# Kernel optimization log

Hardware: AMD Instinct MI355X
Metric: run time of the kernel (lower is better)

The kernel has to match this reference:

```python
import jax, jax.numpy as jnp
import numpy as np

# FlowNetC correlation hyperparameters (init_kwargs)
PAD = 4            # pad_size
KERNEL = 1         # kernel_size (1x1 patch)
MD = 4             # max_displacement
STRIDE1 = 1        # stride over output positions
STRIDE2 = 1        # stride over displacements


def setup_inputs() -> dict:
    key = jax.random.key(0)
    k1, k2 = jax.random.split(key)
    input1 = jax.random.normal(k1, (8, 256, 96, 128), dtype=jnp.float32)
    input2 = jax.random.normal(k2, (8, 256, 96, 128), dtype=jnp.float32)
    return {"input1": input1, "input2": input2}


def reference(input1, input2):
    # Cost volume: out[b, d, y, x] = (1/C) * sum_c input1[b,c,y,x] * input2[b,c,y+dy,x+dx]
    # for all displacements (dy, dx) in [-MD, MD] with step STRIDE2.
    # With pad_size == max_displacement, kernel_size == 1, stride1 == 1 the output
    # spatial grid equals the input grid (FlowNetC configuration). Normalization
    # matches correlation_cuda: sumelems = kernel_size^2 * C.
    B, C, H, W = input1.shape
    p2 = jnp.pad(input2, ((0, 0), (0, 0), (PAD, PAD), (PAD, PAD)))
    disp = range(-MD, MD + 1, STRIDE2)  # 9 offsets -> 81 displacement channels
    outs = []
    for dy in disp:
        for dx in disp:
            shifted = jax.lax.dynamic_slice(p2, (0, 0, PAD + dy, PAD + dx), (B, C, H, W))
            # mean over channels == sum / (KERNEL*KERNEL*C) since KERNEL == 1
            outs.append(jnp.mean(input1 * shifted, axis=1))
    return jnp.stack(outs, axis=1)  # [B, 81, H, W]
```

## Files before the change

kernel.cpp:

```cpp
#include <hip/hip_runtime.h>
#include <hip/hip_bf16.h>


#define B_ 8
#define C_ 256
#define H_ 96
#define W_ 128
#define HW_ 12288
#define CHW_ 3145728

#define IN1_OFF 0
#define IN2_OFF 16384
#define IN2_ROWB (48 * 64)

typedef __attribute__((ext_vector_type(8))) short short8;
typedef __attribute__((ext_vector_type(4))) float f32x4;

__device__ __forceinline__ int swz16(int g, int slot) {
    return (g ^ (slot & 3) ^ ((slot >> 2) & 3)) * 16;
}

__device__ __forceinline__ void stage8(const float* __restrict__ sp, char* dst0, char* dst1) {
    float2 v[8];
    #pragma unroll
    for (int j = 0; j < 8; ++j) v[j] = *(const float2*)(sp + (size_t)j * HW_);
    union { __hip_bfloat162 h2[4]; short8 s8; } u0, u1;
    #pragma unroll
    for (int j = 0; j < 4; ++j) {
        u0.h2[j] = __float22bfloat162_rn(float2{v[2 * j].x, v[2 * j + 1].x});
        u1.h2[j] = __float22bfloat162_rn(float2{v[2 * j].y, v[2 * j + 1].y});
    }
    *(short8*)dst0 = u0.s8;
    *(short8*)dst1 = u1.s8;
}

__global__ __launch_bounds__(1024, 4) void corr_mfma2(
    const float* __restrict__ in1,
    const float* __restrict__ in2,
    float* __restrict__ out)
{
    __shared__ __align__(16) char lds[65536];

    const int tid = threadIdx.x;

    const int blk  = blockIdx.x;
    const int b    = blk & 7;
    const int rest = blk >> 3;
    const int yt   = rest >> 2;
    const int xq   = rest & 3;

    #pragma unroll
    for (int k = 0; k < 4; ++k)
        *(f32x4*)(lds + tid * 16 + k * 16384) = f32x4{0.f, 0.f, 0.f, 0.f};

    const int lane = tid & 63;
    const int wv   = tid >> 6;
    const int xt   = wv & 1;
    const int ut   = (wv >> 1) & 1;
    const int yrh  = wv >> 2;
    const int ln   = lane & 15;
    const int qd   = lane >> 4;

    const int pA   = 16 * xt + ln;
    const int offA0 = IN1_OFF + ((2 * yrh) * 32 + pA) * 64 + swz16(qd, pA);
    const int pB   = 16 * (xt + ut) + ln;
    const int offB = IN2_OFF + ((2 * yrh) * 48 + pB) * 64 + swz16(qd, pB);

    const float* in1b = in1 + (size_t)b * CHW_;
    const float* in2b = in2 + (size_t)b * CHW_;

    f32x4 acc0[9], acc1[9];
    #pragma unroll
    for (int s = 0; s < 9; ++s) { acc0[s] = f32x4{0.f,0.f,0.f,0.f}; acc1[s] = f32x4{0.f,0.f,0.f,0.f}; }

    __syncthreads();

    for (int kc = 0; kc < 8; ++kc) {
        const int ch0 = kc * 32;
        #pragma unroll
        for (int it = 0; it < 2; ++it) {
            const int S = tid + it * 1024;
            if (S < 1536) {
                const int pp = S % 24;
                const int rg = S / 24;
                const int g  = rg & 3;
                const int r  = rg >> 2;
                const int px = pp * 2;
                const int gx = xq * 32 - 8 + px;
                const int ry = yt * 8 - 4 + r;
                if (gx >= 0 && gx <= 126 && ry >= 0 && ry < H_) {
                    const float* sp = in2b + (size_t)(ch0 + 8 * g) * HW_ + ry * W_ + gx;
                    const int slot = r * 48 + px;
                    char* d0 = lds + IN2_OFF + slot * 64 + swz16(g, slot);
                    char* d1 = lds + IN2_OFF + (slot + 1) * 64 + swz16(g, slot + 1);
                    stage8(sp, d0, d1);
                }
            } else {
                const int S1 = S - 1536;
                const int pp = S1 & 15;
                const int rg = S1 >> 4;
                const int g  = rg & 3;
                const int r  = rg >> 2;
                const int px = pp * 2;
                const int gx = xq * 32 + px;
                const int yy = yt * 8 + r;
                const float* sp = in1b + (size_t)(ch0 + 8 * g) * HW_ + yy * W_ + gx;
                const int slot = r * 32 + px;
                char* d0 = lds + IN1_OFF + slot * 64 + swz16(g, slot);
                char* d1 = lds + IN1_OFF + (slot + 1) * 64 + swz16(g, slot + 1);
                stage8(sp, d0, d1);
            }
        }
        __syncthreads();
        short8 a0  = *(const short8*)(lds + offA0);
        short8 a1  = *(const short8*)(lds + offA0 + 32 * 64);
        short8 blo = *(const short8*)(lds + offB);
        #pragma unroll
        for (int s = 0; s < 9; ++s) {
            short8 bhi = *(const short8*)(lds + offB + (s + 1) * IN2_ROWB);
            acc0[s] = __builtin_amdgcn_mfma_f32_16x16x32_bf16(a0, blo, acc0[s], 0, 0, 0);
            acc1[s] = __builtin_amdgcn_mfma_f32_16x16x32_bf16(a1, bhi, acc1[s], 0, 0, 0);
            blo = bhi;
        }
        __syncthreads();
    }

    const float scale = 1.0f / 256.0f;
    const int x0 = xq * 32 + 16 * xt;
    const int ybase = yt * 8 + 2 * yrh;
    #pragma unroll
    for (int s = 0; s < 9; ++s) {
        #pragma unroll
        for (int yr = 0; yr < 2; ++yr) {
            const f32x4 a = yr ? acc1[s] : acc0[s];
            const int y = ybase + yr;
            #pragma unroll
            for (int r = 0; r < 4; ++r) {
                const int m  = qd * 4 + r;
                const int dx = ln - m - 8 + 16 * ut;
                if (dx >= -4 && dx <= 4) {
                    out[(((size_t)b * 81 + (size_t)(s * 9 + dx + 4)) * H_ + y) * W_ + (x0 + m)]
                        = a[r] * scale;
                }
            }
        }
    }
}

extern "C" void kernel_launch(void* const* d_in, const int* in_sizes, int n_in,
                              void* d_out, int out_size, void* d_ws, size_t ws_size,
                              hipStream_t stream) {
    const float* in1 = (const float*)d_in[0];
    const float* in2 = (const float*)d_in[1];
    float* out = (float*)d_out;

    corr_mfma2<<<384, 1024, 0, stream>>>(in1, in2, out);
}
```

Measured before the change: 271.2 us.

## Halve x-tile per block and widen global loads to float4 staging

Shrinks each block's tile from 32 to 16 output columns, launching 768 blocks of 512 threads with a smaller LDS footprint. Staging now loads float4 (four pixels over eight channels) per thread instead of float2, so each thread writes four swizzled LDS slots. The aim is more blocks in flight, better occupancy and wider, more efficient global loads. In exchange the in2 halo overhead per block grows (32 staged columns for 16 outputs), which raises redundant global traffic.

```diff
diff --git a/kernel.cpp b/kernel.cpp
--- a/kernel.cpp
+++ b/kernel.cpp
@@ -10,8 +10,8 @@
 #define CHW_ 3145728
 
 #define IN1_OFF 0
-#define IN2_OFF 16384
-#define IN2_ROWB (48 * 64)
+#define IN2_OFF 8192
+#define IN2_ROWB (32 * 64)
 
 typedef __attribute__((ext_vector_type(8))) short short8;
 typedef __attribute__((ext_vector_type(4))) float f32x4;
@@ -20,54 +20,70 @@
     return (g ^ (slot & 3) ^ ((slot >> 2) & 3)) * 16;
 }
 
-__device__ __forceinline__ void stage8(const float* __restrict__ sp, char* dst0, char* dst1) {
-    float2 v[8];
+__device__ __forceinline__ void stage16(const float* __restrict__ sp, char* __restrict__ base,
+                                        int slot, int g) {
+    f32x4 v[8];
     #pragma unroll
-    for (int j = 0; j < 8; ++j) v[j] = *(const float2*)(sp + (size_t)j * HW_);
-    union { __hip_bfloat162 h2[4]; short8 s8; } u0, u1;
+    for (int j = 0; j < 8; ++j) v[j] = *(const f32x4*)(sp + (size_t)j * HW_);
     #pragma unroll
-    for (int j = 0; j < 4; ++j) {
-        u0.h2[j] = __float22bfloat162_rn(float2{v[2 * j].x, v[2 * j + 1].x});
-        u1.h2[j] = __float22bfloat162_rn(float2{v[2 * j].y, v[2 * j + 1].y});
+    for (int p = 0; p < 4; ++p) {
+        union { __hip_bfloat162 h2[4]; short8 s8; } u;
+        #pragma unroll
+        for (int jj = 0; jj < 4; ++jj)
+            u.h2[jj] = __float22bfloat162_rn(float2{v[2 * jj][p], v[2 * jj + 1][p]});
+        *(short8*)(base + (slot + p) * 64 + swz16(g, slot + p)) = u.s8;
     }
-    *(short8*)dst0 = u0.s8;
-    *(short8*)dst1 = u1.s8;
 }
 
-__global__ __launch_bounds__(1024, 4) void corr_mfma2(
+__global__ __launch_bounds__(512, 4) void corr_mfma3(
     const float* __restrict__ in1,
     const float* __restrict__ in2,
     float* __restrict__ out)
 {
-    __shared__ __align__(16) char lds[65536];
+    __shared__ __align__(16) char lds[40960];
 
     const int tid = threadIdx.x;
 
     const int blk  = blockIdx.x;
     const int b    = blk & 7;
     const int rest = blk >> 3;
-    const int yt   = rest >> 2;
-    const int xq   = rest & 3;
+    const int yt   = rest >> 3;
+    const int xh   = rest & 7;
 
     #pragma unroll
-    for (int k = 0; k < 4; ++k)
-        *(f32x4*)(lds + tid * 16 + k * 16384) = f32x4{0.f, 0.f, 0.f, 0.f};
+    for (int k = 0; k < 5; ++k)
+        *(f32x4*)(lds + tid * 16 + k * 8192) = f32x4{0.f, 0.f, 0.f, 0.f};
 
     const int lane = tid & 63;
     const int wv   = tid >> 6;
-    const int xt   = wv & 1;
-    const int ut   = (wv >> 1) & 1;
-    const int yrh  = wv >> 2;
+    const int ut   = wv & 1;
+    const int yrh  = wv >> 1;
     const int ln   = lane & 15;
     const int qd   = lane >> 4;
 
-    const int pA   = 16 * xt + ln;
-    const int offA0 = IN1_OFF + ((2 * yrh) * 32 + pA) * 64 + swz16(qd, pA);
-    const int pB   = 16 * (xt + ut) + ln;
-    const int offB = IN2_OFF + ((2 * yrh) * 48 + pB) * 64 + swz16(qd, pB);
+    const int offA0 = IN1_OFF + ((2 * yrh) * 16 + ln) * 64 + swz16(qd, ln);
+    const int pB    = 16 * ut + ln;
+    const int offB  = IN2_OFF + ((2 * yrh) * 32 + pB) * 64 + swz16(qd, pB);
 
     const float* in1b = in1 + (size_t)b * CHW_;
     const float* in2b = in2 + (size_t)b * CHW_;
+
+    const int pp2 = tid & 7;
+    const int g2  = (tid >> 3) & 3;
+    const int r2  = tid >> 5;
+    const int px2 = 4 * pp2;
+    const int gx2 = xh * 16 - 8 + px2;
+    const int ry2 = yt * 8 - 4 + r2;
+    const bool valid2 = (gx2 >= 0) && (gx2 <= 124) && (ry2 >= 0) && (ry2 < H_);
+    const int slot2 = r2 * 32 + px2;
+
+    const int pp1 = tid & 3;
+    const int g1  = (tid >> 2) & 3;
+    const int r1  = tid >> 4;
+    const int px1 = 4 * pp1;
+    const int gx1 = xh * 16 + px1;
+    const int y1  = yt * 8 + r1;
+    const int slot1 = r1 * 16 + px1;
 
     f32x4 acc0[9], acc1[9];
     #pragma unroll
@@ -76,44 +92,16 @@
     __syncthreads();
 
     for (int kc = 0; kc < 8; ++kc) {
-        const int ch0 = kc * 32;
-        #pragma unroll
-        for (int it = 0; it < 2; ++it) {
-            const int S = tid + it * 1024;
-            if (S < 1536) {
-                const int pp = S % 24;
-                const int rg = S / 24;
-                const int g  = rg & 3;
-                const int r  = rg >> 2;
-                const int px = pp * 2;
-                const int gx = xq * 32 - 8 + px;
-                const int ry = yt * 8 - 4 + r;
-                if (gx >= 0 && gx <= 126 && ry >= 0 && ry < H_) {
-                    const float* sp = in2b + (size_t)(ch0 + 8 * g) * HW_ + ry * W_ + gx;
-                    const int slot = r * 48 + px;
-                    char* d0 = lds + IN2_OFF + slot * 64 + swz16(g, slot);
-                    char* d1 = lds + IN2_OFF + (slot + 1) * 64 + swz16(g, slot + 1);
-                    stage8(sp, d0, d1);
-                }
-            } else {
-                const int S1 = S - 1536;
-                const int pp = S1 & 15;
-                const int rg = S1 >> 4;
-                const int g  = rg & 3;
-                const int r  = rg >> 2;
-                const int px = pp * 2;
-                const int gx = xq * 32 + px;
-                const int yy = yt * 8 + r;
-                const float* sp = in1b + (size_t)(ch0 + 8 * g) * HW_ + yy * W_ + gx;
-                const int slot = r * 32 + px;
-                char* d0 = lds + IN1_OFF + slot * 64 + swz16(g, slot);
-                char* d1 = lds + IN1_OFF + (slot + 1) * 64 + swz16(g, slot + 1);
-                stage8(sp, d0, d1);
-            }
-        }
+        const size_t choff = (size_t)(kc * 32) * HW_;
+        if (valid2)
+            stage16(in2b + choff + (size_t)(8 * g2) * HW_ + ry2 * W_ + gx2,
+                    lds + IN2_OFF, slot2, g2);
+        if (tid < 128)
+            stage16(in1b + choff + (size_t)(8 * g1) * HW_ + y1 * W_ + gx1,
+                    lds + IN1_OFF, slot1, g1);
         __syncthreads();
         short8 a0  = *(const short8*)(lds + offA0);
-        short8 a1  = *(const short8*)(lds + offA0 + 32 * 64);
+        short8 a1  = *(const short8*)(lds + offA0 + 16 * 64);
         short8 blo = *(const short8*)(lds + offB);
         #pragma unroll
         for (int s = 0; s < 9; ++s) {
@@ -126,7 +114,7 @@
     }
 
     const float scale = 1.0f / 256.0f;
-    const int x0 = xq * 32 + 16 * xt;
+    const int x0 = xh * 16;
     const int ybase = yt * 8 + 2 * yrh;
     #pragma unroll
     for (int s = 0; s < 9; ++s) {
@@ -154,5 +142,5 @@
     const float* in2 = (const float*)d_in[1];
     float* out = (float*)d_out;
 
-    corr_mfma2<<<384, 1024, 0, stream>>>(in1, in2, out);
+    corr_mfma3<<<768, 512, 0, stream>>>(in1, in2, out);
 }
```

After: 262.5 us. 3.2% less time.
